# Performance work log

Hardware: AMD Instinct MI355X
Metric: run time of the kernel (lower is better)

Reference implementation:

```python
import jax, jax.numpy as jnp
import numpy as np
from jax import lax

DIM = 64
D_STATE = 16
D_CONV = 4
EXPAND = 2
D_INNER = EXPAND * DIM  # 128
EPS = 1e-3  # keras LayerNormalization default epsilon


def setup_inputs() -> dict:
    key = jax.random.key(0)
    ks = jax.random.split(key, 9)
    B, H, W, D = 2, 48, 48, 48
    x = jax.random.normal(ks[0], (B, H, W, D, DIM), dtype=jnp.float32)
    # Dense kernels (fan-in scaled), conv kernel is depthwise: [k, 1, d_inner]
    W_in = jax.random.normal(ks[1], (DIM, 2 * D_INNER), jnp.float32) / np.sqrt(DIM)
    conv_w = jax.random.normal(ks[2], (D_CONV, 1, D_INNER), jnp.float32) / np.sqrt(D_CONV)
    conv_b = jnp.zeros((D_INNER,), jnp.float32)
    W_x = jax.random.normal(ks[3], (D_INNER, D_STATE + D_INNER), jnp.float32) / np.sqrt(D_INNER)
    W_dt = jax.random.normal(ks[4], (D_INNER, D_INNER), jnp.float32) / np.sqrt(D_INNER)
    b_dt = jnp.zeros((D_INNER,), jnp.float32)
    W_out = jax.random.normal(ks[5], (D_INNER, DIM), jnp.float32) / np.sqrt(D_INNER)
    gamma = jnp.ones((DIM,), jnp.float32)
    beta = jnp.zeros((DIM,), jnp.float32)
    return {"x": x, "W_in": W_in, "conv_w": conv_w, "conv_b": conv_b,
            "W_x": W_x, "W_dt": W_dt, "b_dt": b_dt, "W_out": W_out,
            "gamma": gamma, "beta": beta}


def _layernorm(z, gamma, beta):
    mu = jnp.mean(z, axis=-1, keepdims=True)
    var = jnp.mean(jnp.square(z - mu), axis=-1, keepdims=True)
    return gamma * (z - mu) * lax.rsqrt(var + EPS) + beta


def reference(x, W_in, conv_w, conv_b, W_x, W_dt, b_dt, W_out, gamma, beta):
    B, H, W, D, C = x.shape
    L = H * W * D
    x_flat = x.reshape(B, L, C)                       # [B, L, C]
    x_and_res = x_flat @ W_in                         # [B, L, 2*d_inner]
    x_ssm, res = jnp.split(x_and_res, 2, axis=-1)     # each [B, L, d_inner]
    # depthwise Conv1D, kernel=4, TF 'same' padding (pad_left=1, pad_right=2)
    x_ssm = lax.conv_general_dilated(
        x_ssm, conv_w, window_strides=(1,), padding=[(1, 2)],
        dimension_numbers=("NWC", "WIO", "NWC"), feature_group_count=D_INNER) + conv_b
    x_ssm = jax.nn.silu(x_ssm)
    # simplified SSM: projections + softplus + cumulative-sum scan over L
    x_proj = x_ssm @ W_x                              # [B, L, d_state+d_inner]
    dt = jax.nn.softplus(x_ssm @ W_dt + b_dt)         # [B, L, d_inner]
    state = jnp.cumsum(x_proj[..., :D_INNER] * dt, axis=1)  # [B, L, d_inner]
    y = state * jax.nn.silu(res)                      # gated output
    out = (y @ W_out).reshape(B, H, W, D, C)
    return _layernorm(out + x, gamma, beta)
```

## Files before the change

### kernel.cpp

```cpp
#include <hip/hip_runtime.h>
#include <hip/hip_bf16.h>
#include <math.h>

#define L_LEN 110592
#define TILE 32
#define NT 3456
#define XROWS (L_LEN + 16)

typedef float  floatx4 __attribute__((ext_vector_type(4)));
typedef short  short8  __attribute__((ext_vector_type(8)));

__device__ __forceinline__ float fast_silu(float v) {
    return v * __builtin_amdgcn_rcpf(1.f + __expf(-v));
}
__device__ __forceinline__ float fast_softplus(float d) {
    return fmaxf(d, 0.f) + __logf(1.f + __expf(-fabsf(d)));
}

__global__ __launch_bounds__(256) void kW_x(const float* __restrict__ x,
                                            __hip_bfloat16* __restrict__ xb)
{
    long idx = (long)blockIdx.x * 256 + threadIdx.x;
    const long total = (long)2 * XROWS * 16;
    if (idx >= total) return;
    const int k4 = (int)(idx & 15) << 2;
    const long rowg = idx >> 4;
    const int b = (int)(rowg / XROWS);
    const long row = rowg - (long)b * XROWS;
    __hip_bfloat16* dst = xb + (rowg << 6) + k4;
    if (row == 0 || row > L_LEN) {
        dst[0] = __float2bfloat16(0.f); dst[1] = __float2bfloat16(0.f);
        dst[2] = __float2bfloat16(0.f); dst[3] = __float2bfloat16(0.f);
    } else {
        const float4 v = *(const float4*)(x + (((long)b * L_LEN + (row - 1)) << 6) + k4);
        dst[0] = __float2bfloat16(v.x); dst[1] = __float2bfloat16(v.y);
        dst[2] = __float2bfloat16(v.z); dst[3] = __float2bfloat16(v.w);
    }
}

__global__ __launch_bounds__(256) void kW_w(
    const float* __restrict__ W_in, const float* __restrict__ W_x,
    const float* __restrict__ W_dt, const float* __restrict__ W_out,
    __hip_bfloat16* __restrict__ wti, __hip_bfloat16* __restrict__ wpt,
    __hip_bfloat16* __restrict__ wtr, __hip_bfloat16* __restrict__ wot)
{
    const int t = threadIdx.x;
    for (int idx = t; idx < 128 * 64; idx += 256) {
        int n = idx >> 6, k = idx & 63;
        wti[idx] = __float2bfloat16(W_in[k * 256 + n]);
        wtr[idx] = __float2bfloat16(W_in[k * 256 + 128 + n]);
    }
    for (int idx = t; idx < 256 * 128; idx += 256) {
        int n = idx >> 7, k = idx & 127;
        float v = (n < 128) ? W_x[k * 144 + n] : W_dt[k * 128 + (n - 128)];
        wpt[idx] = __float2bfloat16(v);
    }
    for (int idx = t; idx < 64 * 128; idx += 256) {
        int n = idx >> 7, k = idx & 127;
        wot[idx] = __float2bfloat16(W_out[k * 64 + n]);
    }
}

__global__ __launch_bounds__(256) void kA(
    const __hip_bfloat16* __restrict__ xb,
    const __hip_bfloat16* __restrict__ wti,
    const __hip_bfloat16* __restrict__ wpt,
    const float* __restrict__ conv_w, const float* __restrict__ conv_b,
    const float* __restrict__ b_dt,
    __hip_bfloat16* __restrict__ s, float* __restrict__ sums)
{
    __shared__ float xs[128 * 52];
    __shared__ __hip_bfloat16 xcb[32 * 136];

    const int t = threadIdx.x;
    const int lane = t & 63;
    const int w = t >> 6;
    const int quad = lane >> 4;
    const int lr = lane & 15;
    const int tile = blockIdx.x;
    const int b = blockIdx.y;
    const int l0 = tile * TILE;

    {
        floatx4 acc[3][2] = {};
        const long xrow0 = (long)b * XROWS + l0;
        #pragma unroll
        for (int ks = 0; ks < 2; ++ks) {
            short8 bfr[2];
            #pragma unroll
            for (int j = 0; j < 2; ++j) {
                const int n = w * 32 + j * 16 + lr;
                bfr[j] = *(const short8*)(wti + (n << 6) + ks * 32 + quad * 8);
            }
            #pragma unroll
            for (int mt = 0; mt < 3; ++mt) {
                short8 afr = *(const short8*)(xb + ((xrow0 + mt * 16 + lr) << 6) + ks * 32 + quad * 8);
                acc[mt][0] = __builtin_amdgcn_mfma_f32_16x16x32_bf16(afr, bfr[0], acc[mt][0], 0, 0, 0);
                acc[mt][1] = __builtin_amdgcn_mfma_f32_16x16x32_bf16(afr, bfr[1], acc[mt][1], 0, 0, 0);
            }
        }
        #pragma unroll
        for (int mt = 0; mt < 3; ++mt)
            #pragma unroll
            for (int j = 0; j < 2; ++j) {
                const int col = w * 32 + j * 16 + lr;
                *(floatx4*)&xs[col * 52 + mt * 16 + quad * 4] = acc[mt][j];
            }
    }
    __syncthreads();

    {
        const int c = t & 127;
        const int m0 = (t >> 7) * 16;
        const float cw0 = conv_w[c], cw1 = conv_w[128 + c];
        const float cw2 = conv_w[256 + c], cw3 = conv_w[384 + c];
        const float cb = conv_b[c];
        float wbuf[20];
        #pragma unroll
        for (int j = 0; j < 5; ++j)
            *(float4*)&wbuf[j * 4] = *(const float4*)&xs[c * 52 + m0 + j * 4];
        #pragma unroll
        for (int i = 0; i < 16; ++i) {
            float v = wbuf[i] * cw0 + wbuf[i + 1] * cw1 + wbuf[i + 2] * cw2
                    + wbuf[i + 3] * cw3 + cb;
            xcb[(m0 + i) * 136 + c] = __float2bfloat16(fast_silu(v));
        }
    }
    __syncthreads();

    {
        floatx4 accx[2][2] = {}, accd[2][2] = {};
        #pragma unroll
        for (int ks = 0; ks < 4; ++ks) {
            short8 afr[2];
            #pragma unroll
            for (int mt = 0; mt < 2; ++mt)
                afr[mt] = *(const short8*)&xcb[(mt * 16 + lr) * 136 + ks * 32 + quad * 8];
            #pragma unroll
            for (int j = 0; j < 2; ++j) {
                const int n = w * 32 + j * 16 + lr;
                short8 bx = *(const short8*)(wpt + (n << 7) + ks * 32 + quad * 8);
                short8 bd = *(const short8*)(wpt + ((n + 128) << 7) + ks * 32 + quad * 8);
                #pragma unroll
                for (int mt = 0; mt < 2; ++mt) {
                    accx[mt][j] = __builtin_amdgcn_mfma_f32_16x16x32_bf16(afr[mt], bx, accx[mt][j], 0, 0, 0);
                    accd[mt][j] = __builtin_amdgcn_mfma_f32_16x16x32_bf16(afr[mt], bd, accd[mt][j], 0, 0, 0);
                }
            }
        }
        const long base = (long)b * L_LEN + l0;
        float ps0 = 0.f, ps1 = 0.f;
        #pragma unroll
        for (int j = 0; j < 2; ++j) {
            const int col = w * 32 + j * 16 + lr;
            const float bdv = b_dt[col];
            float psl = 0.f;
            #pragma unroll
            for (int mt = 0; mt < 2; ++mt) {
                #pragma unroll
                for (int r = 0; r < 4; ++r) {
                    float dv = accd[mt][j][r] + bdv;
                    float sv = accx[mt][j][r] * fast_softplus(dv);
                    __hip_bfloat16 h = __float2bfloat16(sv);
                    s[((base + mt * 16 + quad * 4 + r) << 7) + col] = h;
                    psl += __bfloat162float(h);
                }
            }
            if (j == 0) ps0 = psl; else ps1 = psl;
        }
        ps0 += __shfl_xor(ps0, 16); ps0 += __shfl_xor(ps0, 32);
        ps1 += __shfl_xor(ps1, 16); ps1 += __shfl_xor(ps1, 32);
        const long sb = ((long)b * NT + tile) << 7;
        if (quad == 0)      sums[sb + w * 32 + lr] = ps0;
        else if (quad == 1) sums[sb + w * 32 + 16 + lr] = ps1;
    }
}

#define CHUNK 432
__global__ __launch_bounds__(256) void kB(float* __restrict__ sums)
{
    __shared__ float tls[256];
    const int cc = threadIdx.x & 31;
    const int ct = threadIdx.x >> 5;
    const int cg = blockIdx.x;
    const int b  = blockIdx.y;
    const int c  = cg * 32 + cc;
    const long tbase = ((long)b * NT + (long)ct * CHUNK) * 128 + c;

    float tot = 0.f;
    for (int j = 0; j < CHUNK; j += 8) {
        float v[8];
        #pragma unroll
        for (int k = 0; k < 8; ++k) v[k] = sums[tbase + (long)(j + k) * 128];
        #pragma unroll
        for (int k = 0; k < 8; ++k) tot += v[k];
    }
    tls[ct * 32 + cc] = tot;
    __syncthreads();

    float run = 0.f;
    #pragma unroll
    for (int p = 0; p < 8; ++p)
        if (p < ct) run += tls[p * 32 + cc];

    for (int j = 0; j < CHUNK; j += 8) {
        float v[8];
        #pragma unroll
        for (int k = 0; k < 8; ++k) v[k] = sums[tbase + (long)(j + k) * 128];
        #pragma unroll
        for (int k = 0; k < 8; ++k) {
            sums[tbase + (long)(j + k) * 128] = run;
            run += v[k];
        }
    }
}

__global__ __launch_bounds__(256) void kC(
    const float* __restrict__ x,
    const __hip_bfloat16* __restrict__ xb,
    const __hip_bfloat16* __restrict__ wtr,
    const __hip_bfloat16* __restrict__ wot,
    const float* __restrict__ gamma, const float* __restrict__ beta,
    const __hip_bfloat16* __restrict__ s, const float* __restrict__ offs,
    float* __restrict__ out)
{
    __shared__ float resf[32 * 128];
    __shared__ __hip_bfloat16 ybf[32 * 136];

    const int t = threadIdx.x;
    const int lane = t & 63;
    const int w = t >> 6;
    const int quad = lane >> 4;
    const int lr = lane & 15;
    const int tile = blockIdx.x;
    const int b = blockIdx.y;
    const int l0 = tile * TILE;
    const long base = (long)b * L_LEN;

    {
        floatx4 acc[2][2] = {};
        const long xrow0 = (long)b * XROWS + l0 + 1;
        #pragma unroll
        for (int ks = 0; ks < 2; ++ks) {
            short8 bfr[2];
            #pragma unroll
            for (int j = 0; j < 2; ++j) {
                const int n = w * 32 + j * 16 + lr;
                bfr[j] = *(const short8*)(wtr + (n << 6) + ks * 32 + quad * 8);
            }
            #pragma unroll
            for (int mt = 0; mt < 2; ++mt) {
                short8 afr = *(const short8*)(xb + ((xrow0 + mt * 16 + lr) << 6) + ks * 32 + quad * 8);
                acc[mt][0] = __builtin_amdgcn_mfma_f32_16x16x32_bf16(afr, bfr[0], acc[mt][0], 0, 0, 0);
                acc[mt][1] = __builtin_amdgcn_mfma_f32_16x16x32_bf16(afr, bfr[1], acc[mt][1], 0, 0, 0);
            }
        }
        #pragma unroll
        for (int mt = 0; mt < 2; ++mt)
            #pragma unroll
            for (int j = 0; j < 2; ++j) {
                const int col = w * 32 + j * 16 + lr;
                #pragma unroll
                for (int r = 0; r < 4; ++r) {
                    float v = acc[mt][j][r];
                    resf[(mt * 16 + quad * 4 + r) * 128 + col] = fast_silu(v);
                }
            }
    }
    __syncthreads();

    if (t < 128) {
        float run = offs[((long)b * NT + tile) * 128 + t];
        const __hip_bfloat16* sp = s + ((base + l0) << 7) + t;
        #pragma unroll 8
        for (int q = 0; q < 32; ++q) {
            run += __bfloat162float(sp[q << 7]);
            ybf[q * 136 + t] = __float2bfloat16(resf[q * 128 + t] * run);
        }
    }
    __syncthreads();

    {
        float* zbuf = resf;
        floatx4 acc[2] = {};
        const int n = w * 16 + lr;
        #pragma unroll
        for (int ks = 0; ks < 4; ++ks) {
            short8 bfr = *(const short8*)(wot + (n << 7) + ks * 32 + quad * 8);
            #pragma unroll
            for (int mt = 0; mt < 2; ++mt) {
                short8 afr = *(const short8*)&ybf[(mt * 16 + lr) * 136 + ks * 32 + quad * 8];
                acc[mt] = __builtin_amdgcn_mfma_f32_16x16x32_bf16(afr, bfr, acc[mt], 0, 0, 0);
            }
        }
        __syncthreads();
        #pragma unroll
        for (int mt = 0; mt < 2; ++mt)
            #pragma unroll
            for (int r = 0; r < 4; ++r)
                zbuf[(mt * 16 + quad * 4 + r) * 68 + n] = acc[mt][r];
    }
    __syncthreads();

    {
        const float* zbuf = resf;
        const int d = t & 63;
        const int dg = t >> 6;
        const float g  = gamma[d];
        const float bt = beta[d];
        #pragma unroll 2
        for (int i = 0; i < 8; ++i) {
            int q = dg + 4 * i;
            float z = zbuf[q * 68 + d] + x[(base + l0 + q) * 64 + d];
            float zsum = z;
            #pragma unroll
            for (int off = 32; off > 0; off >>= 1) zsum += __shfl_xor(zsum, off);
            float mu = zsum * 0.015625f;
            float dz = z - mu;
            float vsum = dz * dz;
            #pragma unroll
            for (int off = 32; off > 0; off >>= 1) vsum += __shfl_xor(vsum, off);
            float inv = rsqrtf(vsum * 0.015625f + 1e-3f);
            out[(base + l0 + q) * 64 + d] = g * dz * inv + bt;
        }
    }
}

extern "C" void kernel_launch(void* const* d_in, const int* in_sizes, int n_in,
                              void* d_out, int out_size, void* d_ws, size_t ws_size,
                              hipStream_t stream) {
    const float* x      = (const float*)d_in[0];
    const float* W_in   = (const float*)d_in[1];
    const float* conv_w = (const float*)d_in[2];
    const float* conv_b = (const float*)d_in[3];
    const float* W_x    = (const float*)d_in[4];
    const float* W_dt   = (const float*)d_in[5];
    const float* b_dt   = (const float*)d_in[6];
    const float* W_out  = (const float*)d_in[7];
    const float* gamma  = (const float*)d_in[8];
    const float* beta   = (const float*)d_in[9];
    float* out = (float*)d_out;

    __hip_bfloat16* s    = (__hip_bfloat16*)d_ws;
    float*          sums = (float*)((char*)d_ws + 56623104);
    __hip_bfloat16* xb   = (__hip_bfloat16*)((char*)d_ws + 60162048);
    __hip_bfloat16* wti  = (__hip_bfloat16*)((char*)d_ws + 88477696);
    __hip_bfloat16* wpt  = (__hip_bfloat16*)((char*)d_ws + 88494080);
    __hip_bfloat16* wtr  = (__hip_bfloat16*)((char*)d_ws + 88559616);
    __hip_bfloat16* wot  = (__hip_bfloat16*)((char*)d_ws + 88576000);

    const long xconv_units = (long)2 * XROWS * 16;
    kW_x<<<(int)((xconv_units + 255) / 256), 256, 0, stream>>>(x, xb);
    kW_w<<<1, 256, 0, stream>>>(W_in, W_x, W_dt, W_out, wti, wpt, wtr, wot);
    dim3 grid(NT, 2);
    kA<<<grid, 256, 0, stream>>>(xb, wti, wpt, conv_w, conv_b, b_dt, s, sums);
    dim3 gridB(4, 2);
    kB<<<gridB, 256, 0, stream>>>(sums);
    kC<<<grid, 256, 0, stream>>>(x, xb, wtr, wot, gamma, beta, s, sums, out);
}
```

Before: 321.4 us.

## Fuse x bf16 conversion into GEMM loads and parallelize tile-sum scan

Removes the separate pass that converted x to a padded bf16 copy; kA and kC now read fp32 x directly and pack it to bf16 in registers, with boundary masking for the conv halo. The single 8-block tile-sum scan is replaced by a three-stage hierarchical scan (64 chunks per batch: reduce, scan of chunk totals, per-chunk rescan) to expose more parallelism. The pre-conv projection buffer in shared memory is stored as bf16 instead of fp32 to cut LDS footprint. This trades a full read/write pass over x for twice-as-wide fp32 global loads in both GEMM kernels, adds two kernel launches, and adds extra rounding of the pre-conv values.

After: 317.8 us. Within noise of the previous version (-1.1%).

```diff
diff --git a/kernel.cpp b/kernel.cpp
--- a/kernel.cpp
+++ b/kernel.cpp
@@ -5,10 +5,13 @@
 #define L_LEN 110592
 #define TILE 32
 #define NT 3456
-#define XROWS (L_LEN + 16)
+#define NCH 64
+#define TPC 54
+#define XS_S 60
 
 typedef float  floatx4 __attribute__((ext_vector_type(4)));
 typedef short  short8  __attribute__((ext_vector_type(8)));
+typedef short  short4v __attribute__((ext_vector_type(4)));
 
 __device__ __forceinline__ float fast_silu(float v) {
     return v * __builtin_amdgcn_rcpf(1.f + __expf(-v));
@@ -16,26 +19,19 @@
 __device__ __forceinline__ float fast_softplus(float d) {
     return fmaxf(d, 0.f) + __logf(1.f + __expf(-fabsf(d)));
 }
-
-__global__ __launch_bounds__(256) void kW_x(const float* __restrict__ x,
-                                            __hip_bfloat16* __restrict__ xb)
-{
-    long idx = (long)blockIdx.x * 256 + threadIdx.x;
-    const long total = (long)2 * XROWS * 16;
-    if (idx >= total) return;
-    const int k4 = (int)(idx & 15) << 2;
-    const long rowg = idx >> 4;
-    const int b = (int)(rowg / XROWS);
-    const long row = rowg - (long)b * XROWS;
-    __hip_bfloat16* dst = xb + (rowg << 6) + k4;
-    if (row == 0 || row > L_LEN) {
-        dst[0] = __float2bfloat16(0.f); dst[1] = __float2bfloat16(0.f);
-        dst[2] = __float2bfloat16(0.f); dst[3] = __float2bfloat16(0.f);
-    } else {
-        const float4 v = *(const float4*)(x + (((long)b * L_LEN + (row - 1)) << 6) + k4);
-        dst[0] = __float2bfloat16(v.x); dst[1] = __float2bfloat16(v.y);
-        dst[2] = __float2bfloat16(v.z); dst[3] = __float2bfloat16(v.w);
-    }
+__device__ __forceinline__ short f2bf(float f) {
+    __hip_bfloat16 h = __float2bfloat16(f);
+    return *reinterpret_cast<short*>(&h);
+}
+__device__ __forceinline__ float bf2f(short s) {
+    __hip_bfloat16 h = *reinterpret_cast<__hip_bfloat16*>(&s);
+    return __bfloat162float(h);
+}
+__device__ __forceinline__ short8 pack_bf8(float4 a, float4 b) {
+    short8 r;
+    r[0] = f2bf(a.x); r[1] = f2bf(a.y); r[2] = f2bf(a.z); r[3] = f2bf(a.w);
+    r[4] = f2bf(b.x); r[5] = f2bf(b.y); r[6] = f2bf(b.z); r[7] = f2bf(b.w);
+    return r;
 }
 
 __global__ __launch_bounds__(256) void kW_w(
@@ -62,14 +58,14 @@
 }
 
 __global__ __launch_bounds__(256) void kA(
-    const __hip_bfloat16* __restrict__ xb,
+    const float* __restrict__ x,
     const __hip_bfloat16* __restrict__ wti,
     const __hip_bfloat16* __restrict__ wpt,
     const float* __restrict__ conv_w, const float* __restrict__ conv_b,
     const float* __restrict__ b_dt,
     __hip_bfloat16* __restrict__ s, float* __restrict__ sums)
 {
-    __shared__ float xs[128 * 52];
+    __shared__ __hip_bfloat16 xs[128 * XS_S];
     __shared__ __hip_bfloat16 xcb[32 * 136];
 
     const int t = threadIdx.x;
@@ -83,7 +79,6 @@
 
     {
         floatx4 acc[3][2] = {};
-        const long xrow0 = (long)b * XROWS + l0;
         #pragma unroll
         for (int ks = 0; ks < 2; ++ks) {
             short8 bfr[2];
@@ -94,7 +89,13 @@
             }
             #pragma unroll
             for (int mt = 0; mt < 3; ++mt) {
-                short8 afr = *(const short8*)(xb + ((xrow0 + mt * 16 + lr) << 6) + ks * 32 + quad * 8);
+                const long row = (long)l0 - 1 + mt * 16 + lr;
+                const bool ok = (row >= 0) && (row < L_LEN);
+                const float* xp = x + (((long)b * L_LEN + (ok ? row : 0)) << 6)
+                                    + ks * 32 + quad * 8;
+                float4 u0 = {0.f,0.f,0.f,0.f}, u1 = {0.f,0.f,0.f,0.f};
+                if (ok) { u0 = ((const float4*)xp)[0]; u1 = ((const float4*)xp)[1]; }
+                short8 afr = pack_bf8(u0, u1);
                 acc[mt][0] = __builtin_amdgcn_mfma_f32_16x16x32_bf16(afr, bfr[0], acc[mt][0], 0, 0, 0);
                 acc[mt][1] = __builtin_amdgcn_mfma_f32_16x16x32_bf16(afr, bfr[1], acc[mt][1], 0, 0, 0);
             }
@@ -104,7 +105,10 @@
             #pragma unroll
             for (int j = 0; j < 2; ++j) {
                 const int col = w * 32 + j * 16 + lr;
-                *(floatx4*)&xs[col * 52 + mt * 16 + quad * 4] = acc[mt][j];
+                short4v pk;
+                pk.x = f2bf(acc[mt][j][0]); pk.y = f2bf(acc[mt][j][1]);
+                pk.z = f2bf(acc[mt][j][2]); pk.w = f2bf(acc[mt][j][3]);
+                *(short4v*)&xs[col * XS_S + mt * 16 + quad * 4] = pk;
             }
     }
     __syncthreads();
@@ -115,14 +119,17 @@
         const float cw0 = conv_w[c], cw1 = conv_w[128 + c];
         const float cw2 = conv_w[256 + c], cw3 = conv_w[384 + c];
         const float cb = conv_b[c];
-        float wbuf[20];
-        #pragma unroll
-        for (int j = 0; j < 5; ++j)
-            *(float4*)&wbuf[j * 4] = *(const float4*)&xs[c * 52 + m0 + j * 4];
+        float wb[20];
+        #pragma unroll
+        for (int j = 0; j < 5; ++j) {
+            short4v sv = *(const short4v*)&xs[c * XS_S + m0 + j * 4];
+            wb[j*4+0] = bf2f(sv.x); wb[j*4+1] = bf2f(sv.y);
+            wb[j*4+2] = bf2f(sv.z); wb[j*4+3] = bf2f(sv.w);
+        }
         #pragma unroll
         for (int i = 0; i < 16; ++i) {
-            float v = wbuf[i] * cw0 + wbuf[i + 1] * cw1 + wbuf[i + 2] * cw2
-                    + wbuf[i + 3] * cw3 + cb;
+            float v = wb[i] * cw0 + wb[i + 1] * cw1 + wb[i + 2] * cw2
+                    + wb[i + 3] * cw3 + cb;
             xcb[(m0 + i) * 136 + c] = __float2bfloat16(fast_silu(v));
         }
     }
@@ -176,40 +183,59 @@
     }
 }
 
-#define CHUNK 432
-__global__ __launch_bounds__(256) void kB(float* __restrict__ sums)
-{
-    __shared__ float tls[256];
-    const int cc = threadIdx.x & 31;
-    const int ct = threadIdx.x >> 5;
-    const int cg = blockIdx.x;
-    const int b  = blockIdx.y;
-    const int c  = cg * 32 + cc;
-    const long tbase = ((long)b * NT + (long)ct * CHUNK) * 128 + c;
-
+__global__ __launch_bounds__(256) void kB1(const float* __restrict__ sums,
+                                           float* __restrict__ csum)
+{
+    __shared__ float ps[256];
+    const int t = threadIdx.x;
+    const int c = t & 127, h = t >> 7;
+    const int ch = blockIdx.x, b = blockIdx.y;
+    const long tb = ((long)b * NT + ch * TPC + h * 27) * 128 + c;
     float tot = 0.f;
-    for (int j = 0; j < CHUNK; j += 8) {
+    for (int j = 0; j < 27; j += 9) {
+        float v[9];
+        #pragma unroll
+        for (int k = 0; k < 9; ++k) v[k] = sums[tb + (long)(j + k) * 128];
+        #pragma unroll
+        for (int k = 0; k < 9; ++k) tot += v[k];
+    }
+    ps[t] = tot;
+    __syncthreads();
+    if (t < 128) csum[((long)b * NCH + ch) * 128 + t] = ps[t] + ps[t + 128];
+}
+
+__global__ __launch_bounds__(256) void kB2(float* __restrict__ csum)
+{
+    const int t = threadIdx.x;
+    const int c = t & 127, b = t >> 7;
+    const long base = (long)b * NCH * 128 + c;
+    float run = 0.f;
+    for (int ch = 0; ch < NCH; ch += 8) {
         float v[8];
         #pragma unroll
-        for (int k = 0; k < 8; ++k) v[k] = sums[tbase + (long)(j + k) * 128];
-        #pragma unroll
-        for (int k = 0; k < 8; ++k) tot += v[k];
-    }
-    tls[ct * 32 + cc] = tot;
-    __syncthreads();
-
-    float run = 0.f;
-    #pragma unroll
-    for (int p = 0; p < 8; ++p)
-        if (p < ct) run += tls[p * 32 + cc];
-
-    for (int j = 0; j < CHUNK; j += 8) {
-        float v[8];
-        #pragma unroll
-        for (int k = 0; k < 8; ++k) v[k] = sums[tbase + (long)(j + k) * 128];
+        for (int k = 0; k < 8; ++k) v[k] = csum[base + (long)(ch + k) * 128];
         #pragma unroll
         for (int k = 0; k < 8; ++k) {
-            sums[tbase + (long)(j + k) * 128] = run;
+            csum[base + (long)(ch + k) * 128] = run;
+            run += v[k];
+        }
+    }
+}
+
+__global__ __launch_bounds__(128) void kB3(float* __restrict__ sums,
+                                           const float* __restrict__ csum)
+{
+    const int c = threadIdx.x;
+    const int ch = blockIdx.x, b = blockIdx.y;
+    float run = csum[((long)b * NCH + ch) * 128 + c];
+    const long tb = ((long)b * NT + ch * TPC) * 128 + c;
+    for (int j = 0; j < TPC; j += 9) {
+        float v[9];
+        #pragma unroll
+        for (int k = 0; k < 9; ++k) v[k] = sums[tb + (long)(j + k) * 128];
+        #pragma unroll
+        for (int k = 0; k < 9; ++k) {
+            sums[tb + (long)(j + k) * 128] = run;
             run += v[k];
         }
     }
@@ -217,7 +243,6 @@
 
 __global__ __launch_bounds__(256) void kC(
     const float* __restrict__ x,
-    const __hip_bfloat16* __restrict__ xb,
     const __hip_bfloat16* __restrict__ wtr,
     const __hip_bfloat16* __restrict__ wot,
     const float* __restrict__ gamma, const float* __restrict__ beta,
@@ -239,7 +264,6 @@
 
     {
         floatx4 acc[2][2] = {};
-        const long xrow0 = (long)b * XROWS + l0 + 1;
         #pragma unroll
         for (int ks = 0; ks < 2; ++ks) {
             short8 bfr[2];
@@ -250,7 +274,9 @@
             }
             #pragma unroll
             for (int mt = 0; mt < 2; ++mt) {
-                short8 afr = *(const short8*)(xb + ((xrow0 + mt * 16 + lr) << 6) + ks * 32 + quad * 8);
+                const float* xp = x + ((base + l0 + mt * 16 + lr) << 6) + ks * 32 + quad * 8;
+                float4 u0 = ((const float4*)xp)[0], u1 = ((const float4*)xp)[1];
+                short8 afr = pack_bf8(u0, u1);
                 acc[mt][0] = __builtin_amdgcn_mfma_f32_16x16x32_bf16(afr, bfr[0], acc[mt][0], 0, 0, 0);
                 acc[mt][1] = __builtin_amdgcn_mfma_f32_16x16x32_bf16(afr, bfr[1], acc[mt][1], 0, 0, 0);
             }
@@ -261,10 +287,8 @@
             for (int j = 0; j < 2; ++j) {
                 const int col = w * 32 + j * 16 + lr;
                 #pragma unroll
-                for (int r = 0; r < 4; ++r) {
-                    float v = acc[mt][j][r];
-                    resf[(mt * 16 + quad * 4 + r) * 128 + col] = fast_silu(v);
-                }
+                for (int r = 0; r < 4; ++r)
+                    resf[(mt * 16 + quad * 4 + r) * 128 + col] = fast_silu(acc[mt][j][r]);
             }
     }
     __syncthreads();
@@ -343,18 +367,18 @@
 
     __hip_bfloat16* s    = (__hip_bfloat16*)d_ws;
     float*          sums = (float*)((char*)d_ws + 56623104);
-    __hip_bfloat16* xb   = (__hip_bfloat16*)((char*)d_ws + 60162048);
+    float*          csum = (float*)((char*)d_ws + 60162048);
     __hip_bfloat16* wti  = (__hip_bfloat16*)((char*)d_ws + 88477696);
     __hip_bfloat16* wpt  = (__hip_bfloat16*)((char*)d_ws + 88494080);
     __hip_bfloat16* wtr  = (__hip_bfloat16*)((char*)d_ws + 88559616);
     __hip_bfloat16* wot  = (__hip_bfloat16*)((char*)d_ws + 88576000);
 
-    const long xconv_units = (long)2 * XROWS * 16;
-    kW_x<<<(int)((xconv_units + 255) / 256), 256, 0, stream>>>(x, xb);
     kW_w<<<1, 256, 0, stream>>>(W_in, W_x, W_dt, W_out, wti, wpt, wtr, wot);
     dim3 grid(NT, 2);
-    kA<<<grid, 256, 0, stream>>>(xb, wti, wpt, conv_w, conv_b, b_dt, s, sums);
-    dim3 gridB(4, 2);
-    kB<<<gridB, 256, 0, stream>>>(sums);
-    kC<<<grid, 256, 0, stream>>>(x, xb, wtr, wot, gamma, beta, s, sums, out);
-}
+    kA<<<grid, 256, 0, stream>>>(x, wti, wpt, conv_w, conv_b, b_dt, s, sums);
+    dim3 gridB(NCH, 2);
+    kB1<<<gridB, 256, 0, stream>>>(sums, csum);
+    kB2<<<1, 256, 0, stream>>>(csum);
+    kB3<<<gridB, 128, 0, stream>>>(sums, csum);
+    kC<<<grid, 256, 0, stream>>>(x, wtr, wot, gamma, beta, s, sums, out);
+}
```
